# Performance work log

Measured on AMD Instinct MI355X. Metric: run time of the kernel, lower is better.

## Reference

```python
import jax, jax.numpy as jnp
import numpy as np

N_HEAD = 16
MASK_PENALTY = 10000.0


def setup_inputs() -> dict:
    key = jax.random.key(0)
    k1, k2, k3 = jax.random.split(key, 3)
    B, S, D = 2, 2048, 1024
    x = jax.random.normal(k1, (B, S, D), dtype=jnp.float32)
    w_attn = jax.random.normal(k2, (D, 3 * D), dtype=jnp.float32) * 0.02
    b_attn = jnp.zeros((3 * D,), dtype=jnp.float32)
    w_proj = jax.random.normal(k3, (D, D), dtype=jnp.float32) * 0.02
    b_proj = jnp.zeros((D,), dtype=jnp.float32)
    return {"x": x, "w_attn": w_attn, "b_attn": b_attn, "w_proj": w_proj, "b_proj": b_proj}


def _split_heads(t, n_head):
    B, S, D = t.shape
    return t.reshape(B, S, n_head, D // n_head).transpose(0, 2, 1, 3)  # [B,H,S,dh]


def reference(x, w_attn, b_attn, w_proj, b_proj):
    B, S, D = x.shape
    qkv = x @ w_attn + b_attn  # fused QKV conv1d: [B,S,3D]
    q, k, v = jnp.split(qkv, 3, axis=2)
    q = _split_heads(q, N_HEAD)
    k = _split_heads(k, N_HEAD)
    v = _split_heads(v, N_HEAD)
    dh = D // N_HEAD
    w = jnp.einsum("bhqd,bhkd->bhqk", q, k) / jnp.sqrt(jnp.asarray(dh, dtype=q.dtype))
    # GPT-2 additive causal mask: w*b - 10000*(1-b)
    i = jnp.arange(S)[:, None]
    j = jnp.arange(S)[None, :]
    b = (i >= j).astype(w.dtype)  # nd == ns here
    w = w * b - MASK_PENALTY * (1.0 - b)
    w = jax.nn.softmax(w, axis=-1)
    a = jnp.einsum("bhqk,bhkd->bhqd", w, v)  # [B,H,S,dh]
    a = a.transpose(0, 2, 1, 3).reshape(B, S, D)  # merge heads
    return a @ w_proj + b_proj
```

## Files before the change

kernel.cpp:

```cpp
#include <hip/hip_runtime.h>
#include <hip/hip_bf16.h>


typedef short short8 __attribute__((ext_vector_type(8)));
typedef float f32x4 __attribute__((ext_vector_type(4)));

__device__ __forceinline__ unsigned short f2b(float f) {
    unsigned int x;
    __builtin_memcpy(&x, &f, 4);
    unsigned int r = x + 0x7FFF + ((x >> 16) & 1);
    return (unsigned short)(r >> 16);
}

__device__ __forceinline__ unsigned int pk2(float a, float b) {
    __hip_bfloat162 h = __float22bfloat162_rn(make_float2(a, b));
    unsigned int u;
    __builtin_memcpy(&u, &h, 4);
    return u;
}

__device__ __forceinline__ void load_lds16(const unsigned short* g, unsigned short* l) {
    __builtin_amdgcn_global_load_lds(
        (const __attribute__((address_space(1))) unsigned int*)g,
        (__attribute__((address_space(3))) unsigned int*)l, 16, 0, 0);
}

__global__ __launch_bounds__(256) void prep(const float* __restrict__ x, unsigned int* __restrict__ xb,
                                            const float* __restrict__ wA, unsigned short* __restrict__ wtA,
                                            const float* __restrict__ wP, unsigned short* __restrict__ wtP) {
    const int bx = blockIdx.x, tid = threadIdx.x;
    if (bx < 4096) {
        int i = (bx * 256 + tid) * 4;
        float4 f = *(const float4*)(x + i);
        uint2 p;
        p.x = (unsigned int)f2b(f.x) | ((unsigned int)f2b(f.y) << 16);
        p.y = (unsigned int)f2b(f.z) | ((unsigned int)f2b(f.w) << 16);
        *(uint2*)(xb + i / 2) = p;
        return;
    }
    __shared__ unsigned short t[32][33];
    const float* in;
    unsigned short* out;
    int R, C, gx, gy;
    if (bx < 7168) { int i = bx - 4096; gx = i % 96; gy = i / 96; in = wA; out = wtA; R = 1024; C = 3072; }
    else           { int i = bx - 7168; gx = i % 32; gy = i / 32; in = wP; out = wtP; R = 1024; C = 1024; }
    const int tx = tid & 31, ty = tid >> 5;
    const int c0 = gx * 32, r0 = gy * 32;
#pragma unroll
    for (int i = 0; i < 4; i++)
        t[ty + i * 8][tx] = f2b(in[(r0 + ty + i * 8) * C + c0 + tx]);
    __syncthreads();
#pragma unroll
    for (int i = 0; i < 4; i++)
        out[(c0 + ty + i * 8) * R + r0 + tx] = t[tx][ty + i * 8];
}

__global__ __launch_bounds__(256) void qkv_gemm(const unsigned short* __restrict__ X,
                                                const unsigned short* __restrict__ WT,
                                                const float* __restrict__ bias,
                                                unsigned short* __restrict__ Qo,
                                                unsigned short* __restrict__ Ko,
                                                unsigned short* __restrict__ Vt) {
    __shared__ __align__(16) unsigned short SMEM[8192];
    unsigned short* As = SMEM;
    unsigned short* Bs = SMEM + 4096;
    const int tid = threadIdx.x;
    const int w = tid >> 6, l = tid & 63, l15 = l & 15, quad = l >> 4;
    const int wr = w >> 1, wc = w & 1;
    const int m0 = blockIdx.y * 128, n0 = blockIdx.x * 128;

    const int sr = w * 16 + (l >> 2);
    const int gch = (l & 3) ^ ((l >> 3) & 3);
    const unsigned short* Asrc = X + (size_t)(m0 + sr) * 1024 + gch * 8;
    const unsigned short* Bsrc = WT + (size_t)(n0 + sr) * 1024 + gch * 8;
    const int rswz = (l15 >> 1) & 3;

    f32x4 acc[4][4];
#pragma unroll
    for (int mt = 0; mt < 4; mt++)
#pragma unroll
        for (int nt = 0; nt < 4; nt++) acc[mt][nt] = (f32x4){0.f, 0.f, 0.f, 0.f};

    for (int k0 = 0; k0 < 1024; k0 += 32) {
        __syncthreads();
        load_lds16(Asrc + k0, &As[tid * 8]);
        load_lds16(Asrc + 65536 + k0, &As[2048 + tid * 8]);
        load_lds16(Bsrc + k0, &Bs[tid * 8]);
        load_lds16(Bsrc + 65536 + k0, &Bs[2048 + tid * 8]);
        __syncthreads();

        short8 af[4], bfr[4];
#pragma unroll
        for (int mt = 0; mt < 4; mt++)
            af[mt] = *(const short8*)&As[(wr * 64 + mt * 16 + l15) * 32 + ((quad ^ rswz) * 8)];
#pragma unroll
        for (int nt = 0; nt < 4; nt++)
            bfr[nt] = *(const short8*)&Bs[(wc * 64 + nt * 16 + l15) * 32 + ((quad ^ rswz) * 8)];
#pragma unroll
        for (int mt = 0; mt < 4; mt++)
#pragma unroll
            for (int nt = 0; nt < 4; nt++)
                acc[mt][nt] = __builtin_amdgcn_mfma_f32_16x16x32_bf16(af[mt], bfr[nt], acc[mt][nt], 0, 0, 0);
    }

    const int which = n0 >> 10;
    const int c0 = n0 & 1023;
    float bv[4];
#pragma unroll
    for (int nt = 0; nt < 4; nt++) bv[nt] = bias[n0 + wc * 64 + nt * 16 + l15];

    if (which < 2) {
        const float scale = (which == 1) ? 0.125f : 1.0f;
        unsigned short* dst = (which == 0) ? Qo : Ko;
#pragma unroll
        for (int mt = 0; mt < 4; mt++)
#pragma unroll
            for (int nt = 0; nt < 4; nt++)
#pragma unroll
                for (int r = 0; r < 4; r++) {
                    int mg = m0 + wr * 64 + mt * 16 + quad * 4 + r;
                    int cg = c0 + wc * 64 + nt * 16 + l15;
                    float v = (acc[mt][nt][r] + bv[nt]) * scale;
                    int h = cg >> 6, d = cg & 63;
                    dst[(((size_t)(mg >> 11) * 16 + h) * 2048 + (mg & 2047)) * 64 + d] = f2b(v);
                }
    } else {
        const int b = m0 >> 11, sbase = m0 & 2047, h0 = c0 >> 6;
#pragma unroll
        for (int p = 0; p < 2; p++) {
            __syncthreads();
            if (wc == p) {
#pragma unroll
                for (int mt = 0; mt < 4; mt++)
#pragma unroll
                    for (int nt = 0; nt < 4; nt++)
#pragma unroll
                        for (int r = 0; r < 4; r++) {
                            float v = acc[mt][nt][r] + bv[nt];
                            int d = nt * 16 + l15;
                            int mloc = wr * 64 + mt * 16 + quad * 4 + r;
                            SMEM[d * 128 + (((mloc >> 4) ^ (d & 7)) << 4) + (mloc & 15)] = f2b(v);
                        }
            }
            __syncthreads();
            const int d = tid >> 2, q4 = tid & 3;
            size_t gb = ((size_t)((b * 16 + h0 + p) * 64 + d)) * 2048 + sbase + q4 * 32;
#pragma unroll
            for (int half = 0; half < 2; half++) {
                int mc = q4 * 2 + half;
                const uint4* s = (const uint4*)&SMEM[d * 128 + ((mc ^ (d & 7)) << 4)];
                *(uint4*)(Vt + gb + half * 16) = s[0];
                *(uint4*)(Vt + gb + half * 16 + 8) = s[1];
            }
        }
    }
}

__global__ __launch_bounds__(256) void attn_k(const unsigned short* __restrict__ Q,
                                              const unsigned short* __restrict__ K,
                                              const unsigned short* __restrict__ Vt,
                                              unsigned short* __restrict__ Om) {
    __shared__ __align__(16) unsigned short Ks[2][4096];
    __shared__ __align__(16) unsigned short Vts[2][4096];
    __shared__ __align__(16) unsigned short QP[4096];

    const int tid = threadIdx.x;
    const int w = tid >> 6, l = tid & 63, l15 = l & 15, quad = l >> 4;
    const int bid = blockIdx.x;
    const int qt = 31 - (bid >> 5);
    const int hb = bid & 31;
    const int q0 = qt * 64;
    const unsigned short* Qb = Q + (size_t)hb * 131072;
    const unsigned short* Kb = K + (size_t)hb * 131072;
    const unsigned short* Vb = Vt + (size_t)hb * 131072;

    const int sr = w * 8 + (l >> 3);
    const int gch = (l & 7) ^ (l >> 3);
    const int swz = l15 & 7;

    load_lds16(Qb + (q0 + sr) * 64 + gch * 8, &QP[tid * 8]);
    load_lds16(Qb + (q0 + 32 + sr) * 64 + gch * 8, &QP[2048 + tid * 8]);
    load_lds16(Kb + sr * 64 + gch * 8, &Ks[0][tid * 8]);
    load_lds16(Kb + (32 + sr) * 64 + gch * 8, &Ks[0][2048 + tid * 8]);
    load_lds16(Vb + sr * 2048 + gch * 8, &Vts[0][tid * 8]);
    load_lds16(Vb + (32 + sr) * 2048 + gch * 8, &Vts[0][2048 + tid * 8]);
    __syncthreads();

    short8 qf[2];
#pragma unroll
    for (int ks = 0; ks < 2; ks++)
        qf[ks] = *(const short8*)&QP[(w * 16 + l15) * 64 + (((ks * 4 + quad) ^ swz) << 3)];

    short8 ones;
#pragma unroll
    for (int j = 0; j < 8; j++) ones[j] = (short)0x3F80;

    f32x4 o[4], lacc;
#pragma unroll
    for (int nt = 0; nt < 4; nt++) o[nt] = (f32x4){0.f, 0.f, 0.f, 0.f};
    lacc = (f32x4){0.f, 0.f, 0.f, 0.f};

    for (int kt = 0; kt <= qt; kt++) {
        const int c = kt & 1;
        __syncthreads();
        if (kt < qt) {
            const int kn = (kt + 1) * 64;
            load_lds16(Kb + (kn + sr) * 64 + gch * 8, &Ks[1 - c][tid * 8]);
            load_lds16(Kb + (kn + 32 + sr) * 64 + gch * 8, &Ks[1 - c][2048 + tid * 8]);
            load_lds16(Vb + sr * 2048 + kn + gch * 8, &Vts[1 - c][tid * 8]);
            load_lds16(Vb + (32 + sr) * 2048 + kn + gch * 8, &Vts[1 - c][2048 + tid * 8]);
        }

        f32x4 sa[4];
#pragma unroll
        for (int nt = 0; nt < 4; nt++) sa[nt] = (f32x4){0.f, 0.f, 0.f, 0.f};
#pragma unroll
        for (int ks = 0; ks < 2; ks++)
#pragma unroll
            for (int nt = 0; nt < 4; nt++) {
                short8 kf = *(const short8*)&Ks[c][(nt * 16 + l15) * 64 + (((ks * 4 + quad) ^ swz) << 3)];
                sa[nt] = __builtin_amdgcn_mfma_f32_16x16x32_bf16(qf[ks], kf, sa[nt], 0, 0, 0);
            }

        float pv[4][4];
        if (kt == qt) {
#pragma unroll
            for (int nt = 0; nt < 4; nt++)
#pragma unroll
                for (int r = 0; r < 4; r++) {
                    bool ok = (nt * 16 + l15) <= (w * 16 + quad * 4 + r);
                    pv[nt][r] = ok ? __expf(sa[nt][r]) : 0.f;
                }
        } else {
#pragma unroll
            for (int nt = 0; nt < 4; nt++)
#pragma unroll
                for (int r = 0; r < 4; r++)
                    pv[nt][r] = __expf(sa[nt][r]);
        }

        const int rb = w * 16 + quad * 4;
#pragma unroll
        for (int nt = 0; nt < 4; nt++) {
            const int col = nt * 16 + l15, ch = col >> 3, wi = col & 7;
#pragma unroll
            for (int rp = 0; rp < 4; rp += 2) {
                unsigned int u = pk2(pv[nt][rp], pv[nt][rp + 1]);
                const int ra = rb + rp, rbn = ra + 1;
                QP[ra * 64 + ((ch ^ (ra & 7)) << 3) + wi] = (unsigned short)(u & 0xffff);
                QP[rbn * 64 + ((ch ^ (rbn & 7)) << 3) + wi] = (unsigned short)(u >> 16);
            }
        }
        asm volatile("s_waitcnt lgkmcnt(0)" ::: "memory");

#pragma unroll
        for (int ks = 0; ks < 2; ks++) {
            short8 pf = *(const short8*)&QP[(w * 16 + l15) * 64 + (((ks * 4 + quad) ^ swz) << 3)];
            lacc = __builtin_amdgcn_mfma_f32_16x16x32_bf16(pf, ones, lacc, 0, 0, 0);
#pragma unroll
            for (int nt = 0; nt < 4; nt++) {
                short8 vf = *(const short8*)&Vts[c][(nt * 16 + l15) * 64 + (((ks * 4 + quad) ^ swz) << 3)];
                o[nt] = __builtin_amdgcn_mfma_f32_16x16x32_bf16(pf, vf, o[nt], 0, 0, 0);
            }
        }
    }

    float inv[4];
#pragma unroll
    for (int r = 0; r < 4; r++) inv[r] = 1.0f / lacc[r];
    const int b = hb >> 4, h = hb & 15;
#pragma unroll
    for (int nt = 0; nt < 4; nt++)
#pragma unroll
        for (int r = 0; r < 4; r++) {
            int sg = q0 + w * 16 + quad * 4 + r;
            int col = h * 64 + nt * 16 + l15;
            Om[((size_t)(b * 2048 + sg)) * 1024 + col] = f2b(o[nt][r] * inv[r]);
        }
}

__global__ __launch_bounds__(256) void proj_gemm(const unsigned short* __restrict__ A,
                                                 const unsigned short* __restrict__ WT,
                                                 const float* __restrict__ bias,
                                                 float* __restrict__ out) {
    __shared__ __align__(16) unsigned short As[128 * 32];
    __shared__ __align__(16) unsigned short Bs[64 * 32];
    const int tid = threadIdx.x;
    const int w = tid >> 6, l = tid & 63, l15 = l & 15, quad = l >> 4;
    const int wr = w >> 1, wc = w & 1;
    const int m0 = blockIdx.y * 128, n0 = blockIdx.x * 64;

    const int sr = w * 16 + (l >> 2);
    const int gch = (l & 3) ^ ((l >> 3) & 3);
    const unsigned short* Asrc = A + (size_t)(m0 + sr) * 1024 + gch * 8;
    const unsigned short* Bsrc = WT + (size_t)(n0 + sr) * 1024 + gch * 8;
    const int rswz = (l15 >> 1) & 3;

    f32x4 acc[4][2];
#pragma unroll
    for (int mt = 0; mt < 4; mt++)
#pragma unroll
        for (int nt = 0; nt < 2; nt++) acc[mt][nt] = (f32x4){0.f, 0.f, 0.f, 0.f};

    for (int k0 = 0; k0 < 1024; k0 += 32) {
        __syncthreads();
        load_lds16(Asrc + k0, &As[tid * 8]);
        load_lds16(Asrc + 65536 + k0, &As[2048 + tid * 8]);
        load_lds16(Bsrc + k0, &Bs[tid * 8]);
        __syncthreads();

        short8 af[4], bfr[2];
#pragma unroll
        for (int mt = 0; mt < 4; mt++)
            af[mt] = *(const short8*)&As[(wr * 64 + mt * 16 + l15) * 32 + ((quad ^ rswz) * 8)];
#pragma unroll
        for (int nt = 0; nt < 2; nt++)
            bfr[nt] = *(const short8*)&Bs[(wc * 32 + nt * 16 + l15) * 32 + ((quad ^ rswz) * 8)];
#pragma unroll
        for (int mt = 0; mt < 4; mt++)
#pragma unroll
            for (int nt = 0; nt < 2; nt++)
                acc[mt][nt] = __builtin_amdgcn_mfma_f32_16x16x32_bf16(af[mt], bfr[nt], acc[mt][nt], 0, 0, 0);
    }

#pragma unroll
    for (int mt = 0; mt < 4; mt++)
#pragma unroll
        for (int nt = 0; nt < 2; nt++)
#pragma unroll
            for (int r = 0; r < 4; r++) {
                int mg = m0 + wr * 64 + mt * 16 + quad * 4 + r;
                int ng = n0 + wc * 32 + nt * 16 + l15;
                out[(size_t)mg * 1024 + ng] = acc[mt][nt][r] + bias[ng];
            }
}

extern "C" void kernel_launch(void* const* d_in, const int* in_sizes, int n_in,
                              void* d_out, int out_size, void* d_ws, size_t ws_size,
                              hipStream_t stream) {
    (void)in_sizes; (void)n_in; (void)out_size; (void)ws_size;
    const float* x      = (const float*)d_in[0];
    const float* w_attn = (const float*)d_in[1];
    const float* b_attn = (const float*)d_in[2];
    const float* w_proj = (const float*)d_in[3];
    const float* b_proj = (const float*)d_in[4];
    float* out = (float*)d_out;
    unsigned short* ws = (unsigned short*)d_ws;

    unsigned short* wtA  = ws;
    unsigned short* wtP  = wtA + 3145728;
    unsigned short* Qw   = wtP + 1048576;
    unsigned short* Kw   = Qw + 4194304;
    unsigned short* Vtw  = Kw + 4194304;
    unsigned short* XbOm = Vtw + 4194304;

    prep<<<8192, 256, 0, stream>>>(x, (unsigned int*)XbOm, w_attn, wtA, w_proj, wtP);
    qkv_gemm<<<dim3(24, 32), 256, 0, stream>>>(XbOm, wtA, b_attn, Qw, Kw, Vtw);
    attn_k<<<1024, 256, 0, stream>>>(Qw, Kw, Vtw, XbOm);
    proj_gemm<<<dim3(16, 32), 256, 0, stream>>>(XbOm, wtP, b_proj, out);
}
```

Before: 189.8 us.

## Double-buffer GEMM LDS tiles and split attention waves across query and key halves

Both GEMM kernels (QKV and projection) now double-buffer their LDS tiles: the next K-slice is prefetched while the current one is consumed, leaving one barrier per iteration instead of two. The attention kernel changes its wave layout from four waves of 16 query rows each to a 2x2 grid of 32 query rows by 32 keys per wave. This halves the K and V fragment reads from LDS per wave, and P is written with packed 64-bit stores. The partial outputs and row sums from the two key-half waves are combined through LDS at the end. The costs are more LDS space, more accumulator registers, and an extra reduction and barrier in the epilogue.

```diff
diff --git a/kernel.cpp b/kernel.cpp
--- a/kernel.cpp
+++ b/kernel.cpp
@@ -61,9 +61,9 @@
                                                 unsigned short* __restrict__ Qo,
                                                 unsigned short* __restrict__ Ko,
                                                 unsigned short* __restrict__ Vt) {
-    __shared__ __align__(16) unsigned short SMEM[8192];
-    unsigned short* As = SMEM;
-    unsigned short* Bs = SMEM + 4096;
+    __shared__ __align__(16) unsigned short SM[16384];
+    unsigned short* As = SM;
+    unsigned short* Bs = SM + 8192;
     const int tid = threadIdx.x;
     const int w = tid >> 6, l = tid & 63, l15 = l & 15, quad = l >> 4;
     const int wr = w >> 1, wc = w & 1;
@@ -81,21 +81,29 @@
 #pragma unroll
         for (int nt = 0; nt < 4; nt++) acc[mt][nt] = (f32x4){0.f, 0.f, 0.f, 0.f};
 
+    load_lds16(Asrc, &As[tid * 8]);
+    load_lds16(Asrc + 65536, &As[2048 + tid * 8]);
+    load_lds16(Bsrc, &Bs[tid * 8]);
+    load_lds16(Bsrc + 65536, &Bs[2048 + tid * 8]);
+
     for (int k0 = 0; k0 < 1024; k0 += 32) {
+        const int c = (k0 >> 5) & 1;
         __syncthreads();
-        load_lds16(Asrc + k0, &As[tid * 8]);
-        load_lds16(Asrc + 65536 + k0, &As[2048 + tid * 8]);
-        load_lds16(Bsrc + k0, &Bs[tid * 8]);
-        load_lds16(Bsrc + 65536 + k0, &Bs[2048 + tid * 8]);
-        __syncthreads();
+        if (k0 + 32 < 1024) {
+            const int pc = 1 - c;
+            load_lds16(Asrc + k0 + 32, &As[pc * 4096 + tid * 8]);
+            load_lds16(Asrc + 65536 + k0 + 32, &As[pc * 4096 + 2048 + tid * 8]);
+            load_lds16(Bsrc + k0 + 32, &Bs[pc * 4096 + tid * 8]);
+            load_lds16(Bsrc + 65536 + k0 + 32, &Bs[pc * 4096 + 2048 + tid * 8]);
+        }
 
         short8 af[4], bfr[4];
 #pragma unroll
         for (int mt = 0; mt < 4; mt++)
-            af[mt] = *(const short8*)&As[(wr * 64 + mt * 16 + l15) * 32 + ((quad ^ rswz) * 8)];
+            af[mt] = *(const short8*)&As[c * 4096 + (wr * 64 + mt * 16 + l15) * 32 + ((quad ^ rswz) * 8)];
 #pragma unroll
         for (int nt = 0; nt < 4; nt++)
-            bfr[nt] = *(const short8*)&Bs[(wc * 64 + nt * 16 + l15) * 32 + ((quad ^ rswz) * 8)];
+            bfr[nt] = *(const short8*)&Bs[c * 4096 + (wc * 64 + nt * 16 + l15) * 32 + ((quad ^ rswz) * 8)];
 #pragma unroll
         for (int mt = 0; mt < 4; mt++)
 #pragma unroll
@@ -139,7 +147,7 @@
                             float v = acc[mt][nt][r] + bv[nt];
                             int d = nt * 16 + l15;
                             int mloc = wr * 64 + mt * 16 + quad * 4 + r;
-                            SMEM[d * 128 + (((mloc >> 4) ^ (d & 7)) << 4) + (mloc & 15)] = f2b(v);
+                            SM[d * 128 + (((mloc >> 4) ^ (d & 7)) << 4) + (mloc & 15)] = f2b(v);
                         }
             }
             __syncthreads();
@@ -148,7 +156,7 @@
 #pragma unroll
             for (int half = 0; half < 2; half++) {
                 int mc = q4 * 2 + half;
-                const uint4* s = (const uint4*)&SMEM[d * 128 + ((mc ^ (d & 7)) << 4)];
+                const uint4* s = (const uint4*)&SM[d * 128 + ((mc ^ (d & 7)) << 4)];
                 *(uint4*)(Vt + gb + half * 16) = s[0];
                 *(uint4*)(Vt + gb + half * 16 + 8) = s[1];
             }
@@ -160,12 +168,14 @@
                                               const unsigned short* __restrict__ K,
                                               const unsigned short* __restrict__ Vt,
                                               unsigned short* __restrict__ Om) {
-    __shared__ __align__(16) unsigned short Ks[2][4096];
-    __shared__ __align__(16) unsigned short Vts[2][4096];
-    __shared__ __align__(16) unsigned short QP[4096];
+    __shared__ __align__(16) unsigned short SM[20480];
+    unsigned short* Ks0 = SM;
+    unsigned short* Vts0 = SM + 8192;
+    unsigned short* QP = SM + 16384;
 
     const int tid = threadIdx.x;
     const int w = tid >> 6, l = tid & 63, l15 = l & 15, quad = l >> 4;
+    const int wq = w >> 1, ws = w & 1;
     const int bid = blockIdx.x;
     const int qt = 31 - (bid >> 5);
     const int hb = bid & 31;
@@ -176,115 +186,161 @@
 
     const int sr = w * 8 + (l >> 3);
     const int gch = (l & 7) ^ (l >> 3);
-    const int swz = l15 & 7;
+    const int swz7 = l15 & 7;
 
     load_lds16(Qb + (q0 + sr) * 64 + gch * 8, &QP[tid * 8]);
     load_lds16(Qb + (q0 + 32 + sr) * 64 + gch * 8, &QP[2048 + tid * 8]);
-    load_lds16(Kb + sr * 64 + gch * 8, &Ks[0][tid * 8]);
-    load_lds16(Kb + (32 + sr) * 64 + gch * 8, &Ks[0][2048 + tid * 8]);
-    load_lds16(Vb + sr * 2048 + gch * 8, &Vts[0][tid * 8]);
-    load_lds16(Vb + (32 + sr) * 2048 + gch * 8, &Vts[0][2048 + tid * 8]);
+    load_lds16(Kb + sr * 64 + gch * 8, &Ks0[tid * 8]);
+    load_lds16(Kb + (32 + sr) * 64 + gch * 8, &Ks0[2048 + tid * 8]);
+    load_lds16(Vb + sr * 2048 + gch * 8, &Vts0[tid * 8]);
+    load_lds16(Vb + (32 + sr) * 2048 + gch * 8, &Vts0[2048 + tid * 8]);
     __syncthreads();
 
-    short8 qf[2];
-#pragma unroll
-    for (int ks = 0; ks < 2; ks++)
-        qf[ks] = *(const short8*)&QP[(w * 16 + l15) * 64 + (((ks * 4 + quad) ^ swz) << 3)];
+    short8 qf[2][2];
+#pragma unroll
+    for (int qnt = 0; qnt < 2; qnt++)
+#pragma unroll
+        for (int ks = 0; ks < 2; ks++)
+            qf[qnt][ks] = *(const short8*)&QP[(wq * 32 + qnt * 16 + l15) * 64 + (((ks * 4 + quad) ^ swz7) << 3)];
 
     short8 ones;
 #pragma unroll
     for (int j = 0; j < 8; j++) ones[j] = (short)0x3F80;
 
-    f32x4 o[4], lacc;
-#pragma unroll
-    for (int nt = 0; nt < 4; nt++) o[nt] = (f32x4){0.f, 0.f, 0.f, 0.f};
-    lacc = (f32x4){0.f, 0.f, 0.f, 0.f};
+    f32x4 o[2][4], lacc[2];
+#pragma unroll
+    for (int pmt = 0; pmt < 2; pmt++) {
+        lacc[pmt] = (f32x4){0.f, 0.f, 0.f, 0.f};
+#pragma unroll
+        for (int dnt = 0; dnt < 4; dnt++) o[pmt][dnt] = (f32x4){0.f, 0.f, 0.f, 0.f};
+    }
 
     for (int kt = 0; kt <= qt; kt++) {
         const int c = kt & 1;
+        const unsigned short* Ksc = Ks0 + c * 4096;
+        const unsigned short* Vtsc = Vts0 + c * 4096;
         __syncthreads();
         if (kt < qt) {
-            const int kn = (kt + 1) * 64;
-            load_lds16(Kb + (kn + sr) * 64 + gch * 8, &Ks[1 - c][tid * 8]);
-            load_lds16(Kb + (kn + 32 + sr) * 64 + gch * 8, &Ks[1 - c][2048 + tid * 8]);
-            load_lds16(Vb + sr * 2048 + kn + gch * 8, &Vts[1 - c][tid * 8]);
-            load_lds16(Vb + (32 + sr) * 2048 + kn + gch * 8, &Vts[1 - c][2048 + tid * 8]);
-        }
-
-        f32x4 sa[4];
-#pragma unroll
-        for (int nt = 0; nt < 4; nt++) sa[nt] = (f32x4){0.f, 0.f, 0.f, 0.f};
-#pragma unroll
-        for (int ks = 0; ks < 2; ks++)
-#pragma unroll
-            for (int nt = 0; nt < 4; nt++) {
-                short8 kf = *(const short8*)&Ks[c][(nt * 16 + l15) * 64 + (((ks * 4 + quad) ^ swz) << 3)];
-                sa[nt] = __builtin_amdgcn_mfma_f32_16x16x32_bf16(qf[ks], kf, sa[nt], 0, 0, 0);
+            const int kn = (kt + 1) * 64, pc = 1 - c;
+            load_lds16(Kb + (kn + sr) * 64 + gch * 8, &Ks0[pc * 4096 + tid * 8]);
+            load_lds16(Kb + (kn + 32 + sr) * 64 + gch * 8, &Ks0[pc * 4096 + 2048 + tid * 8]);
+            load_lds16(Vb + sr * 2048 + kn + gch * 8, &Vts0[pc * 4096 + tid * 8]);
+            load_lds16(Vb + (32 + sr) * 2048 + kn + gch * 8, &Vts0[pc * 4096 + 2048 + tid * 8]);
+        }
+
+        f32x4 sa[2][2];
+#pragma unroll
+        for (int smt = 0; smt < 2; smt++)
+#pragma unroll
+            for (int qnt = 0; qnt < 2; qnt++) sa[smt][qnt] = (f32x4){0.f, 0.f, 0.f, 0.f};
+#pragma unroll
+        for (int ks = 0; ks < 2; ks++) {
+            short8 kf[2];
+#pragma unroll
+            for (int smt = 0; smt < 2; smt++)
+                kf[smt] = *(const short8*)&Ksc[(ws * 32 + smt * 16 + l15) * 64 + (((ks * 4 + quad) ^ swz7) << 3)];
+#pragma unroll
+            for (int smt = 0; smt < 2; smt++)
+#pragma unroll
+                for (int qnt = 0; qnt < 2; qnt++)
+                    sa[smt][qnt] = __builtin_amdgcn_mfma_f32_16x16x32_bf16(kf[smt], qf[qnt][ks], sa[smt][qnt], 0, 0, 0);
+        }
+
+        float pv[2][2][4];
+        if (kt == qt) {
+#pragma unroll
+            for (int smt = 0; smt < 2; smt++)
+#pragma unroll
+                for (int qnt = 0; qnt < 2; qnt++)
+#pragma unroll
+                    for (int r = 0; r < 4; r++) {
+                        int cg = kt * 64 + ws * 32 + smt * 16 + quad * 4 + r;
+                        int rg = q0 + wq * 32 + qnt * 16 + l15;
+                        pv[smt][qnt][r] = (cg <= rg) ? __expf(sa[smt][qnt][r]) : 0.f;
+                    }
+        } else {
+#pragma unroll
+            for (int smt = 0; smt < 2; smt++)
+#pragma unroll
+                for (int qnt = 0; qnt < 2; qnt++)
+#pragma unroll
+                    for (int r = 0; r < 4; r++)
+                        pv[smt][qnt][r] = __expf(sa[smt][qnt][r]);
+        }
+
+#pragma unroll
+        for (int smt = 0; smt < 2; smt++)
+#pragma unroll
+            for (int qnt = 0; qnt < 2; qnt++) {
+                int q = wq * 32 + qnt * 16 + l15;
+                int sb = ws * 32 + smt * 16 + quad * 4;
+                int ch = (sb >> 3) ^ (q & 7);
+                int a16 = q * 64 + (ch << 3) + (sb & 7);
+                uint2 u;
+                u.x = pk2(pv[smt][qnt][0], pv[smt][qnt][1]);
+                u.y = pk2(pv[smt][qnt][2], pv[smt][qnt][3]);
+                *(uint2*)&QP[a16] = u;
             }
-
-        float pv[4][4];
-        if (kt == qt) {
-#pragma unroll
-            for (int nt = 0; nt < 4; nt++)
+        asm volatile("s_waitcnt lgkmcnt(0)" ::: "memory");
+
+        short8 pf[2];
+#pragma unroll
+        for (int pmt = 0; pmt < 2; pmt++) {
+            pf[pmt] = *(const short8*)&QP[(wq * 32 + pmt * 16 + l15) * 64 + (((ws * 4 + quad) ^ swz7) << 3)];
+            lacc[pmt] = __builtin_amdgcn_mfma_f32_16x16x32_bf16(pf[pmt], ones, lacc[pmt], 0, 0, 0);
+        }
+#pragma unroll
+        for (int dnt = 0; dnt < 4; dnt++) {
+            short8 vf = *(const short8*)&Vtsc[(dnt * 16 + l15) * 64 + (((ws * 4 + quad) ^ swz7) << 3)];
+#pragma unroll
+            for (int pmt = 0; pmt < 2; pmt++)
+                o[pmt][dnt] = __builtin_amdgcn_mfma_f32_16x16x32_bf16(pf[pmt], vf, o[pmt][dnt], 0, 0, 0);
+        }
+    }
+
+    __syncthreads();
+    float* red = (float*)SM;
+    float* myp = red + (wq * 64 + l) * 41;
+    if (ws == 1) {
+#pragma unroll
+        for (int pmt = 0; pmt < 2; pmt++) {
+#pragma unroll
+            for (int dnt = 0; dnt < 4; dnt++)
+#pragma unroll
+                for (int r = 0; r < 4; r++) myp[pmt * 16 + dnt * 4 + r] = o[pmt][dnt][r];
+#pragma unroll
+            for (int r = 0; r < 4; r++) myp[32 + pmt * 4 + r] = lacc[pmt][r];
+        }
+    }
+    __syncthreads();
+    if (ws == 0) {
+        float inv[2][4];
+#pragma unroll
+        for (int pmt = 0; pmt < 2; pmt++)
+#pragma unroll
+            for (int r = 0; r < 4; r++)
+                inv[pmt][r] = 1.0f / (lacc[pmt][r] + myp[32 + pmt * 4 + r]);
+        const int b = hb >> 4, h = hb & 15;
+#pragma unroll
+        for (int pmt = 0; pmt < 2; pmt++)
+#pragma unroll
+            for (int dnt = 0; dnt < 4; dnt++)
 #pragma unroll
                 for (int r = 0; r < 4; r++) {
-                    bool ok = (nt * 16 + l15) <= (w * 16 + quad * 4 + r);
-                    pv[nt][r] = ok ? __expf(sa[nt][r]) : 0.f;
+                    float val = (o[pmt][dnt][r] + myp[pmt * 16 + dnt * 4 + r]) * inv[pmt][r];
+                    int sg = q0 + wq * 32 + pmt * 16 + quad * 4 + r;
+                    int col = h * 64 + dnt * 16 + l15;
+                    Om[((size_t)(b * 2048 + sg)) * 1024 + col] = f2b(val);
                 }
-        } else {
-#pragma unroll
-            for (int nt = 0; nt < 4; nt++)
-#pragma unroll
-                for (int r = 0; r < 4; r++)
-                    pv[nt][r] = __expf(sa[nt][r]);
-        }
-
-        const int rb = w * 16 + quad * 4;
-#pragma unroll
-        for (int nt = 0; nt < 4; nt++) {
-            const int col = nt * 16 + l15, ch = col >> 3, wi = col & 7;
-#pragma unroll
-            for (int rp = 0; rp < 4; rp += 2) {
-                unsigned int u = pk2(pv[nt][rp], pv[nt][rp + 1]);
-                const int ra = rb + rp, rbn = ra + 1;
-                QP[ra * 64 + ((ch ^ (ra & 7)) << 3) + wi] = (unsigned short)(u & 0xffff);
-                QP[rbn * 64 + ((ch ^ (rbn & 7)) << 3) + wi] = (unsigned short)(u >> 16);
-            }
-        }
-        asm volatile("s_waitcnt lgkmcnt(0)" ::: "memory");
-
-#pragma unroll
-        for (int ks = 0; ks < 2; ks++) {
-            short8 pf = *(const short8*)&QP[(w * 16 + l15) * 64 + (((ks * 4 + quad) ^ swz) << 3)];
-            lacc = __builtin_amdgcn_mfma_f32_16x16x32_bf16(pf, ones, lacc, 0, 0, 0);
-#pragma unroll
-            for (int nt = 0; nt < 4; nt++) {
-                short8 vf = *(const short8*)&Vts[c][(nt * 16 + l15) * 64 + (((ks * 4 + quad) ^ swz) << 3)];
-                o[nt] = __builtin_amdgcn_mfma_f32_16x16x32_bf16(pf, vf, o[nt], 0, 0, 0);
-            }
-        }
-    }
-
-    float inv[4];
-#pragma unroll
-    for (int r = 0; r < 4; r++) inv[r] = 1.0f / lacc[r];
-    const int b = hb >> 4, h = hb & 15;
-#pragma unroll
-    for (int nt = 0; nt < 4; nt++)
-#pragma unroll
-        for (int r = 0; r < 4; r++) {
-            int sg = q0 + w * 16 + quad * 4 + r;
-            int col = h * 64 + nt * 16 + l15;
-            Om[((size_t)(b * 2048 + sg)) * 1024 + col] = f2b(o[nt][r] * inv[r]);
-        }
+    }
 }
 
 __global__ __launch_bounds__(256) void proj_gemm(const unsigned short* __restrict__ A,
                                                  const unsigned short* __restrict__ WT,
                                                  const float* __restrict__ bias,
                                                  float* __restrict__ out) {
-    __shared__ __align__(16) unsigned short As[128 * 32];
-    __shared__ __align__(16) unsigned short Bs[64 * 32];
+    __shared__ __align__(16) unsigned short As[2][4096];
+    __shared__ __align__(16) unsigned short Bs[2][2048];
     const int tid = threadIdx.x;
     const int w = tid >> 6, l = tid & 63, l15 = l & 15, quad = l >> 4;
     const int wr = w >> 1, wc = w & 1;
@@ -302,20 +358,27 @@
 #pragma unroll
         for (int nt = 0; nt < 2; nt++) acc[mt][nt] = (f32x4){0.f, 0.f, 0.f, 0.f};
 
+    load_lds16(Asrc, &As[0][tid * 8]);
+    load_lds16(Asrc + 65536, &As[0][2048 + tid * 8]);
+    load_lds16(Bsrc, &Bs[0][tid * 8]);
+
     for (int k0 = 0; k0 < 1024; k0 += 32) {
+        const int c = (k0 >> 5) & 1;
         __syncthreads();
-        load_lds16(Asrc + k0, &As[tid * 8]);
-        load_lds16(Asrc + 65536 + k0, &As[2048 + tid * 8]);
-        load_lds16(Bsrc + k0, &Bs[tid * 8]);
-        __syncthreads();
+        if (k0 + 32 < 1024) {
+            const int pc = 1 - c;
+            load_lds16(Asrc + k0 + 32, &As[pc][tid * 8]);
+            load_lds16(Asrc + 65536 + k0 + 32, &As[pc][2048 + tid * 8]);
+            load_lds16(Bsrc + k0 + 32, &Bs[pc][tid * 8]);
+        }
 
         short8 af[4], bfr[2];
 #pragma unroll
         for (int mt = 0; mt < 4; mt++)
-            af[mt] = *(const short8*)&As[(wr * 64 + mt * 16 + l15) * 32 + ((quad ^ rswz) * 8)];
+            af[mt] = *(const short8*)&As[c][(wr * 64 + mt * 16 + l15) * 32 + ((quad ^ rswz) * 8)];
 #pragma unroll
         for (int nt = 0; nt < 2; nt++)
-            bfr[nt] = *(const short8*)&Bs[(wc * 32 + nt * 16 + l15) * 32 + ((quad ^ rswz) * 8)];
+            bfr[nt] = *(const short8*)&Bs[c][(wc * 32 + nt * 16 + l15) * 32 + ((quad ^ rswz) * 8)];
 #pragma unroll
         for (int mt = 0; mt < 4; mt++)
 #pragma unroll
```

Measured after the change: 171.9 us. 9.5% less time.
